# Kernel tuning notes

Hardware: AMD Instinct MI355X
Metric: run time of the kernel (lower is better)

The kernel has to match this reference:

```python
import jax, jax.numpy as jnp
import numpy as np

B, N, HD = 2, 2048, 2048
NH, KVH = 16, 4
D = HD // NH          # 128
R = NH // KVH         # 4 (kv_ratio)
KVD = KVH * D         # 512


def setup_inputs() -> dict:
    key = jax.random.key(0)
    ks = jax.random.split(key, 6)
    s = 0.02
    return {
        "tokens": jax.random.normal(ks[0], (B, N, HD), jnp.float32),
        "norm_w": jnp.ones((HD,), jnp.float32),
        "Wq": jax.random.normal(ks[1], (HD, HD), jnp.float32) * s,
        "bq": jnp.zeros((HD,), jnp.float32),
        "Wk": jax.random.normal(ks[2], (KVD, HD), jnp.float32) * s,
        "bk": jnp.zeros((KVD,), jnp.float32),
        "Wv": jax.random.normal(ks[3], (KVD, HD), jnp.float32) * s,
        "bv": jnp.zeros((KVD,), jnp.float32),
        "Wo": jax.random.normal(ks[4], (HD, HD), jnp.float32) * s,
        "bo": jnp.zeros((HD,), jnp.float32),
    }


def reference(tokens, norm_w, Wq, bq, Wk, bk, Wv, bv, Wo, bo):
    # RMSNorm (torch default eps=None -> finfo eps), learnable weight
    eps = jnp.finfo(tokens.dtype).eps
    x = tokens * jax.lax.rsqrt(jnp.mean(tokens * tokens, axis=-1, keepdims=True) + eps) * norm_w

    # projections -> [B, heads, N, D]
    q = (x @ Wq.T + bq).reshape(B, N, NH, D).transpose(0, 2, 1, 3)
    k = (x @ Wk.T + bk).reshape(B, N, KVH, D).transpose(0, 2, 1, 3)
    v = (x @ Wv.T + bv).reshape(B, N, KVH, D).transpose(0, 2, 1, 3)

    # GQA via tiling the kv block (matches torch.cat of copies: head h uses kv head h % KVH)
    k = jnp.tile(k, (1, R, 1, 1))
    v = jnp.tile(v, (1, R, 1, 1))

    # Faithful (inverted) mask: True where j <= i, and True positions are masked out.
    mask = jnp.arange(N)[None, :] <= jnp.arange(N)[:, None]  # [N, N]

    # No 1/sqrt(D) scaling in the original
    scores = jnp.einsum('bhid,bhjd->bhij', q, k)
    scores = jnp.where(mask[None, None, :, :], jnp.float32(-1e9), scores)
    attn = jax.nn.softmax(scores, axis=-1)

    a = jnp.einsum('bhij,bhjd->bhid', attn, v)       # [B, NH, N, D]
    a = a.transpose(0, 2, 1, 3).reshape(B, N, HD)    # [B, N, HD]
    return a @ Wo.T + bo
```

## Files before the change

### kernel.cpp

```cpp
#include <hip/hip_runtime.h>

#define BB   2
#define NN   2048
#define HDIM 2048
#define NHD  16
#define KVHD 4
#define DD   128
#define KVW  1024
#define MTOK (BB*NN)

typedef _Float16 h8 __attribute__((ext_vector_type(8)));
typedef _Float16 h4 __attribute__((ext_vector_type(4)));
typedef float    f4 __attribute__((ext_vector_type(4)));
typedef float    fx16 __attribute__((ext_vector_type(16)));
typedef short    b8 __attribute__((ext_vector_type(8)));

static __device__ __forceinline__ f4 mfma16(h8 a, h8 b, f4 c) {
    return __builtin_amdgcn_mfma_f32_16x16x32_f16(a, b, c, 0, 0, 0);
}
static __device__ __forceinline__ fx16 mfma32b(b8 a, b8 b, fx16 c) {
    return __builtin_amdgcn_mfma_f32_32x32x16_bf16(a, b, c, 0, 0, 0);
}

static __device__ __forceinline__ unsigned short f2bf(float f) {
    unsigned int u = __float_as_uint(f);
    u += 0x7FFF + ((u >> 16) & 1);
    return (unsigned short)(u >> 16);
}

static __device__ __forceinline__ void gload_lds16(const void* g, void* l) {
    __builtin_amdgcn_global_load_lds(
        (const __attribute__((address_space(1))) void*)g,
        (__attribute__((address_space(3))) void*)l, 16, 0, 0);
}

__global__ __launch_bounds__(256) void rmsnorm_k(const float* __restrict__ t,
                                                 const float* __restrict__ wn,
                                                 _Float16* __restrict__ xh) {
    const int row = blockIdx.x, tid = threadIdx.x;
    const float* rp = t + (size_t)row * HDIM;
    float4 v[2];
    float ss = 0.f;
    #pragma unroll
    for (int p = 0; p < 2; ++p) {
        float4 x = *(const float4*)(rp + (p * 256 + tid) * 4);
        v[p] = x;
        ss += x.x * x.x + x.y * x.y + x.z * x.z + x.w * x.w;
    }
    #pragma unroll
    for (int off = 32; off; off >>= 1) ss += __shfl_xor(ss, off, 64);
    __shared__ float sred[4];
    if ((tid & 63) == 0) sred[tid >> 6] = ss;
    __syncthreads();
    float rs = rsqrtf((sred[0] + sred[1] + sred[2] + sred[3]) * (1.0f / HDIM)
                      + 1.1920928955078125e-07f);
    _Float16* op = xh + (size_t)row * HDIM;
    #pragma unroll
    for (int p = 0; p < 2; ++p) {
        int base = (p * 256 + tid) * 4;
        float4 w = *(const float4*)(wn + base);
        h4 o;
        o[0] = (_Float16)(v[p].x * rs * w.x);
        o[1] = (_Float16)(v[p].y * rs * w.y);
        o[2] = (_Float16)(v[p].z * rs * w.z);
        o[3] = (_Float16)(v[p].w * rs * w.w);
        *(h4*)(op + base) = o;
    }
}

__global__ __launch_bounds__(256) void cvt_k(const float* __restrict__ src,
                                             _Float16* __restrict__ dst, int n) {
    int i = (blockIdx.x * 256 + threadIdx.x) * 4;
    if (i < n) {
        float4 v = *(const float4*)(src + i);
        h4 o; o[0] = (_Float16)v.x; o[1] = (_Float16)v.y;
        o[2] = (_Float16)v.z; o[3] = (_Float16)v.w;
        *(h4*)(dst + i) = o;
    }
}

__global__ void biascat_k(const float* __restrict__ bk, const float* __restrict__ bv,
                          float* __restrict__ bkv, float* __restrict__ vsum) {
    int i = blockIdx.x * 256 + threadIdx.x;
    bkv[i] = (i < 512) ? bk[i] : bv[i - 512];
    vsum[i] = 0.f;
}

__global__ __launch_bounds__(256) void vtrans_k(const _Float16* __restrict__ kv,
                                                unsigned short* __restrict__ vt) {
    const int tid = threadIdx.x;
    const int tok = blockIdx.x * 64 + (tid & 63);
    const int kvh = blockIdx.y;
    const int d0 = (tid >> 6) * 32;
    const int b = tok >> 11, n = tok & (NN - 1);
    const _Float16* src = kv + (size_t)tok * KVW + 512 + kvh * DD + d0;
    unsigned short* dstb = vt + ((size_t)(b * KVHD + kvh) * DD) * NN + n;
    #pragma unroll
    for (int u = 0; u < 4; ++u) {
        h8 v = *(const h8*)(src + u * 8);
        #pragma unroll
        for (int e = 0; e < 8; ++e)
            dstb[(size_t)(d0 + u * 8 + e) * NN] = f2bf((float)v[e]);
    }
}

template <int OUTF32>
__global__ __launch_bounds__(256, 2) void gemm_bt(const _Float16* __restrict__ A,
                                                  const _Float16* __restrict__ Bw,
                                                  const float* __restrict__ bias,
                                                  void* __restrict__ Cout,
                                                  int Ndim, int K) {
    __shared__ _Float16 sA[128 * 64];
    __shared__ _Float16 sB[128 * 64];
    const int tid = threadIdx.x;
    const int lane = tid & 63, w = tid >> 6;
    const int ln = lane & 15, quad = lane >> 4;
    const int wm = w >> 1, wn = w & 1;
    const int m0 = blockIdx.y * 128, n0 = blockIdx.x * 128;

    f4 acc[4][4] = {};
    for (int k0 = 0; k0 < K; k0 += 64) {
        #pragma unroll
        for (int it = 0; it < 4; ++it) {
            int chunk = it * 256 + tid;
            int row = chunk >> 3, p = chunk & 7;
            int c = p ^ (row & 7);
            gload_lds16(A + (size_t)(m0 + row) * K + k0 + c * 8, sA + chunk * 8);
            gload_lds16(Bw + (size_t)(n0 + row) * K + k0 + c * 8, sB + chunk * 8);
        }
        __syncthreads();
        #pragma unroll
        for (int kk = 0; kk < 2; ++kk) {
            h8 af[4], bf[4];
            #pragma unroll
            for (int mt = 0; mt < 4; ++mt)
                af[mt] = *(const h8*)&sA[(wm * 64 + mt * 16 + ln) * 64 +
                                         (((kk * 4 + quad) ^ (ln & 7)) << 3)];
            #pragma unroll
            for (int nt = 0; nt < 4; ++nt)
                bf[nt] = *(const h8*)&sB[(wn * 64 + nt * 16 + ln) * 64 +
                                         (((kk * 4 + quad) ^ (ln & 7)) << 3)];
            #pragma unroll
            for (int mt = 0; mt < 4; ++mt)
                #pragma unroll
                for (int nt = 0; nt < 4; ++nt)
                    acc[mt][nt] = mfma16(af[mt], bf[nt], acc[mt][nt]);
        }
        __syncthreads();
    }
    #pragma unroll
    for (int mt = 0; mt < 4; ++mt) {
        int rowb = m0 + wm * 64 + mt * 16 + quad * 4;
        #pragma unroll
        for (int nt = 0; nt < 4; ++nt) {
            int col = n0 + wn * 64 + nt * 16 + ln;
            float bv = bias[col];
            #pragma unroll
            for (int r = 0; r < 4; ++r) {
                float v = acc[mt][nt][r] + bv;
                if (OUTF32)
                    ((float*)Cout)[(size_t)(rowb + r) * Ndim + col] = v;
                else
                    ((_Float16*)Cout)[(size_t)(rowb + r) * Ndim + col] = (_Float16)v;
            }
        }
    }
}

__global__ __launch_bounds__(256, 2) void attn_k(const _Float16* __restrict__ qh,
                                                 const _Float16* __restrict__ kvp,
                                                 const unsigned short* __restrict__ vt,
                                                 _Float16* __restrict__ ah) {
    __shared__ _Float16 s_k[2][64 * 128];
    __shared__ unsigned short s_v[2][128 * 64];
    __shared__ unsigned short s_p[4][32 * 32];
    const int tid = threadIdx.x;
    const int lane = tid & 63, w = tid >> 6;
    const int ln = lane & 15, quad = lane >> 4;
    const int l5 = lane & 31, hi = lane >> 5;
    const int h = blockIdx.y, b = blockIdx.z;
    const int it0 = b ? (15 - (int)blockIdx.x) : (int)blockIdx.x;
    const int i0 = it0 * 128;
    const int kvh = h & 3;

    h8 qf[2][4];
    #pragma unroll
    for (int t = 0; t < 2; ++t) {
        const _Float16* qrow =
            qh + ((size_t)(b * NN + i0 + w * 32 + t * 16 + ln)) * HDIM + h * DD;
        #pragma unroll
        for (int kc = 0; kc < 4; ++kc)
            qf[t][kc] = *(const h8*)(qrow + kc * 32 + quad * 8);
    }

    b8 ones;
    #pragma unroll
    for (int e = 0; e < 8; ++e) ones[e] = (short)0x3F80;

    fx16 O[4] = {};
    fx16 OS = {};

    auto stage = [&](int jt, int bufi) {
        const int j0s = jt * 64;
        #pragma unroll
        for (int itr = 0; itr < 4; ++itr) {
            int chunk = itr * 256 + tid;
            int jj = chunk >> 4, p = chunk & 15;
            int c = p ^ (jj & 15);
            gload_lds16(kvp + ((size_t)(b * NN + j0s + jj)) * KVW + kvh * DD + c * 8,
                        &s_k[bufi][chunk * 8]);
        }
        #pragma unroll
        for (int itr = 0; itr < 4; ++itr) {
            int chunk = itr * 256 + tid;
            int d = chunk >> 3, p = chunk & 7;
            int c = p ^ (d & 7);
            gload_lds16(vt + ((size_t)(b * KVHD + kvh) * DD + d) * NN + j0s + c * 8,
                        &s_v[bufi][chunk * 8]);
        }
    };

    const int jt0 = it0 * 2;
    stage(jt0, 0);
    for (int jt = jt0; jt < 32; ++jt) {
        const int j0 = jt * 64;
        const int cur = (jt - jt0) & 1;
        __syncthreads();
        if (jt + 1 < 32) stage(jt + 1, cur ^ 1);

        f4 sc[2][4] = {};
        #pragma unroll
        for (int nt = 0; nt < 4; ++nt)
            #pragma unroll
            for (int kc = 0; kc < 4; ++kc) {
                h8 kf = *(const h8*)&s_k[cur][(nt * 16 + ln) * 128 +
                                              (((kc * 4 + quad) ^ ln) << 3)];
                sc[0][nt] = mfma16(kf, qf[0][kc], sc[0][nt]);
                sc[1][nt] = mfma16(kf, qf[1][kc], sc[1][nt]);
            }

        const bool need_mask = (jt < jt0 + 2);
        #pragma unroll
        for (int half = 0; half < 2; ++half) {
            #pragma unroll
            for (int t = 0; t < 2; ++t)
                #pragma unroll
                for (int nn = 0; nn < 2; ++nn) {
                    int nt = half * 2 + nn;
                    float pv[4];
                    #pragma unroll
                    for (int r = 0; r < 4; ++r) {
                        float s = sc[t][nt][r];
                        if (need_mask) {
                            int ig = i0 + w * 32 + t * 16 + ln;
                            int jg = j0 + nt * 16 + quad * 4 + r;
                            if (jg <= ig) s = -1e9f;
                        }
                        pv[r] = __expf(s);
                    }
                    unsigned int u0 = f2bf(pv[0]) | ((unsigned int)f2bf(pv[1]) << 16);
                    unsigned int u1 = f2bf(pv[2]) | ((unsigned int)f2bf(pv[3]) << 16);
                    int addr = (t * 16 + ln) * 32 +
                               (((nn * 2 + (quad >> 1)) ^ (ln & 3)) << 3) +
                               ((quad & 1) << 2);
                    *(uint2*)&s_p[w][addr] = make_uint2(u0, u1);
                }
            #pragma unroll
            for (int ks = 0; ks < 2; ++ks) {
                b8 ap = *(const b8*)&s_p[w][l5 * 32 +
                                            (((ks * 2 + hi) ^ (l5 & 3)) << 3)];
                #pragma unroll
                for (int nt4 = 0; nt4 < 4; ++nt4) {
                    b8 bv = *(const b8*)&s_v[cur][(nt4 * 32 + l5) * 64 +
                                                  (((half * 4 + ks * 2 + hi) ^ (l5 & 7)) << 3)];
                    O[nt4] = mfma32b(ap, bv, O[nt4]);
                }
                OS = mfma32b(ap, ones, OS);
            }
        }
    }

    float inv_l[16];
    #pragma unroll
    for (int rg = 0; rg < 16; ++rg) inv_l[rg] = 1.0f / OS[rg];
    #pragma unroll
    for (int nt4 = 0; nt4 < 4; ++nt4)
        #pragma unroll
        for (int rg = 0; rg < 16; ++rg) {
            int q = (rg & 3) + 8 * (rg >> 2) + 4 * hi;
            ah[((size_t)(b * NN + i0 + w * 32 + q)) * HDIM + h * DD + nt4 * 32 + l5] =
                (_Float16)(O[nt4][rg] * inv_l[rg]);
        }
}

__global__ __launch_bounds__(256) void vsum_k(const _Float16* __restrict__ kvp,
                                              float* __restrict__ vsum) {
    __shared__ float red[16][128];
    const int seg = blockIdx.x, kvh = blockIdx.y, b = blockIdx.z;
    const int tid = threadIdx.x;
    const int jj = tid >> 4, dc = (tid & 15) * 8;
    float acc[8] = {};
    #pragma unroll 4
    for (int j = seg * 256 + jj; j < seg * 256 + 256; j += 16) {
        h8 v = *(const h8*)(kvp + ((size_t)(b * NN + j)) * KVW + 512 + kvh * DD + dc);
        #pragma unroll
        for (int e = 0; e < 8; ++e) acc[e] += (float)v[e];
    }
    #pragma unroll
    for (int e = 0; e < 8; ++e) red[jj][dc + e] = acc[e];
    __syncthreads();
    if (tid < 128) {
        float s = 0.f;
        #pragma unroll
        for (int t = 0; t < 16; ++t) s += red[t][tid];
        atomicAdd(&vsum[(b * KVHD + kvh) * DD + tid], s);
    }
}

__global__ void fixup_write_k(const float* __restrict__ vsum,
                              _Float16* __restrict__ ah) {
    int b = blockIdx.x >> 2, kvh = blockIdx.x & 3, d = threadIdx.x;
    float mean = vsum[(b * KVHD + kvh) * DD + d] * (1.0f / NN);
    #pragma unroll
    for (int r = 0; r < 4; ++r) {
        int h = r * 4 + kvh;
        ah[((size_t)(b * NN + NN - 1)) * HDIM + h * DD + d] = (_Float16)mean;
    }
}

extern "C" void kernel_launch(void* const* d_in, const int* in_sizes, int n_in,
                              void* d_out, int out_size, void* d_ws, size_t ws_size,
                              hipStream_t stream) {
    const float* tokens = (const float*)d_in[0];
    const float* norm_w = (const float*)d_in[1];
    const float* Wq = (const float*)d_in[2];
    const float* bq = (const float*)d_in[3];
    const float* Wk = (const float*)d_in[4];
    const float* bk = (const float*)d_in[5];
    const float* Wv = (const float*)d_in[6];
    const float* bv = (const float*)d_in[7];
    const float* Wo = (const float*)d_in[8];
    const float* bo = (const float*)d_in[9];
    float* out = (float*)d_out;

    char* ws = (char*)d_ws;
    _Float16* x_h   = (_Float16*)(ws);
    _Float16* wq_h  = (_Float16*)(ws + 16777216);
    _Float16* wkv_h = (_Float16*)(ws + 25165824);
    _Float16* wo_h  = (_Float16*)(ws + 29360128);
    float*    bkv   = (float*)   (ws + 37748736);
    _Float16* q_h   = (_Float16*)(ws + 37752832);
    _Float16* kv_h  = (_Float16*)(ws + 54530048);
    _Float16* a_h   = (_Float16*)(ws + 62918656);
    unsigned short* vt_h = (unsigned short*)(ws + 79695872);
    float*    vsum  = (float*)   (ws + 81793024);

    rmsnorm_k<<<MTOK, 256, 0, stream>>>(tokens, norm_w, x_h);
    cvt_k<<<4096, 256, 0, stream>>>(Wq, wq_h, HDIM * HDIM);
    cvt_k<<<1024, 256, 0, stream>>>(Wk, wkv_h, 512 * HDIM);
    cvt_k<<<1024, 256, 0, stream>>>(Wv, wkv_h + 512 * HDIM, 512 * HDIM);
    cvt_k<<<4096, 256, 0, stream>>>(Wo, wo_h, HDIM * HDIM);
    biascat_k<<<4, 256, 0, stream>>>(bk, bv, bkv, vsum);

    gemm_bt<0><<<dim3(HDIM / 128, MTOK / 128), 256, 0, stream>>>(
        x_h, wq_h, bq, (void*)q_h, HDIM, HDIM);
    gemm_bt<0><<<dim3(KVW / 128, MTOK / 128), 256, 0, stream>>>(
        x_h, wkv_h, bkv, (void*)kv_h, KVW, HDIM);

    vtrans_k<<<dim3(MTOK / 64, KVHD), 256, 0, stream>>>(kv_h, vt_h);

    attn_k<<<dim3(16, NHD, BB), 256, 0, stream>>>(q_h, kv_h, vt_h, a_h);
    vsum_k<<<dim3(8, KVHD, BB), 256, 0, stream>>>(kv_h, vsum);
    fixup_write_k<<<BB * KVHD, 128, 0, stream>>>(vsum, a_h);

    gemm_bt<1><<<dim3(HDIM / 128, MTOK / 128), 256, 0, stream>>>(
        a_h, wo_h, bo, (void*)out, HDIM, HDIM);
}
```

Baseline: 319.6 us.

## Build P MFMA operands in registers via lane shuffles instead of LDS round-trip

The attention kernel no longer writes the exponentiated bf16 score tile to a per-wave shared buffer and reads it back as the A operand of the 32x32 MFMA. It packs probabilities in registers and exchanges half of them across lanes with a 16-lane xor shuffle to form the operand layout directly. It also reorders the P·V loop over 16-column key blocks. This removes LDS stores and loads and frees shared memory, at the cost of extra shuffles and selects. The vsum workspace offset also moves.

```diff
diff --git a/kernel.cpp b/kernel.cpp
--- a/kernel.cpp
+++ b/kernel.cpp
@@ -14,6 +14,7 @@
 typedef float    f4 __attribute__((ext_vector_type(4)));
 typedef float    fx16 __attribute__((ext_vector_type(16)));
 typedef short    b8 __attribute__((ext_vector_type(8)));
+typedef unsigned int u4v __attribute__((ext_vector_type(4)));
 
 static __device__ __forceinline__ f4 mfma16(h8 a, h8 b, f4 c) {
     return __builtin_amdgcn_mfma_f32_16x16x32_f16(a, b, c, 0, 0, 0);
@@ -173,11 +174,11 @@
                                                  _Float16* __restrict__ ah) {
     __shared__ _Float16 s_k[2][64 * 128];
     __shared__ unsigned short s_v[2][128 * 64];
-    __shared__ unsigned short s_p[4][32 * 32];
     const int tid = threadIdx.x;
     const int lane = tid & 63, w = tid >> 6;
     const int ln = lane & 15, quad = lane >> 4;
     const int l5 = lane & 31, hi = lane >> 5;
+    const int sel = quad & 1;
     const int h = blockIdx.y, b = blockIdx.z;
     const int it0 = b ? (15 - (int)blockIdx.x) : (int)blockIdx.x;
     const int i0 = it0 * 128;
@@ -240,43 +241,54 @@
             }
 
         const bool need_mask = (jt < jt0 + 2);
-        #pragma unroll
-        for (int half = 0; half < 2; ++half) {
-            #pragma unroll
-            for (int t = 0; t < 2; ++t)
-                #pragma unroll
-                for (int nn = 0; nn < 2; ++nn) {
-                    int nt = half * 2 + nn;
-                    float pv[4];
-                    #pragma unroll
-                    for (int r = 0; r < 4; ++r) {
-                        float s = sc[t][nt][r];
-                        if (need_mask) {
-                            int ig = i0 + w * 32 + t * 16 + ln;
-                            int jg = j0 + nt * 16 + quad * 4 + r;
-                            if (jg <= ig) s = -1e9f;
-                        }
-                        pv[r] = __expf(s);
-                    }
-                    unsigned int u0 = f2bf(pv[0]) | ((unsigned int)f2bf(pv[1]) << 16);
-                    unsigned int u1 = f2bf(pv[2]) | ((unsigned int)f2bf(pv[3]) << 16);
-                    int addr = (t * 16 + ln) * 32 +
-                               (((nn * 2 + (quad >> 1)) ^ (ln & 3)) << 3) +
-                               ((quad & 1) << 2);
-                    *(uint2*)&s_p[w][addr] = make_uint2(u0, u1);
+        unsigned int u0[4][2], u1[4][2];
+        #pragma unroll
+        for (int nt = 0; nt < 4; ++nt)
+            #pragma unroll
+            for (int rr = 0; rr < 2; ++rr) {
+                float a0 = sc[0][nt][2 * rr], a1 = sc[0][nt][2 * rr + 1];
+                float c0 = sc[1][nt][2 * rr], c1 = sc[1][nt][2 * rr + 1];
+                if (need_mask) {
+                    int jg = j0 + nt * 16 + quad * 4 + 2 * rr;
+                    int ig0 = i0 + w * 32 + ln;
+                    int ig1 = ig0 + 16;
+                    if (jg <= ig0) a0 = -1e9f;
+                    if (jg + 1 <= ig0) a1 = -1e9f;
+                    if (jg <= ig1) c0 = -1e9f;
+                    if (jg + 1 <= ig1) c1 = -1e9f;
                 }
-            #pragma unroll
-            for (int ks = 0; ks < 2; ++ks) {
-                b8 ap = *(const b8*)&s_p[w][l5 * 32 +
-                                            (((ks * 2 + hi) ^ (l5 & 3)) << 3)];
-                #pragma unroll
-                for (int nt4 = 0; nt4 < 4; ++nt4) {
-                    b8 bv = *(const b8*)&s_v[cur][(nt4 * 32 + l5) * 64 +
-                                                  (((half * 4 + ks * 2 + hi) ^ (l5 & 7)) << 3)];
-                    O[nt4] = mfma32b(ap, bv, O[nt4]);
-                }
-                OS = mfma32b(ap, ones, OS);
+                u0[nt][rr] = (unsigned int)f2bf(__expf(a0)) |
+                             ((unsigned int)f2bf(__expf(a1)) << 16);
+                u1[nt][rr] = (unsigned int)f2bf(__expf(c0)) |
+                             ((unsigned int)f2bf(__expf(c1)) << 16);
             }
+
+        b8 paf[4];
+        #pragma unroll
+        for (int nt = 0; nt < 4; ++nt) {
+            unsigned int own0 = sel ? u1[nt][0] : u0[nt][0];
+            unsigned int own1 = sel ? u1[nt][1] : u0[nt][1];
+            unsigned int oth0 = sel ? u0[nt][0] : u1[nt][0];
+            unsigned int oth1 = sel ? u0[nt][1] : u1[nt][1];
+            unsigned int r0 = __shfl_xor(oth0, 16, 64);
+            unsigned int r1 = __shfl_xor(oth1, 16, 64);
+            u4v pw;
+            pw[0] = sel ? r0 : own0;
+            pw[1] = sel ? r1 : own1;
+            pw[2] = sel ? own0 : r0;
+            pw[3] = sel ? own1 : r1;
+            paf[nt] = __builtin_bit_cast(b8, pw);
+        }
+
+        #pragma unroll
+        for (int nt = 0; nt < 4; ++nt) {
+            #pragma unroll
+            for (int dblk = 0; dblk < 4; ++dblk) {
+                b8 bv = *(const b8*)&s_v[cur][(dblk * 32 + l5) * 64 +
+                                              (((nt * 2 + hi) ^ (l5 & 7)) << 3)];
+                O[dblk] = mfma32b(paf[nt], bv, O[dblk]);
+            }
+            OS = mfma32b(paf[nt], ones, OS);
         }
     }
 
@@ -353,7 +365,7 @@
     _Float16* kv_h  = (_Float16*)(ws + 54530048);
     _Float16* a_h   = (_Float16*)(ws + 62918656);
     unsigned short* vt_h = (unsigned short*)(ws + 79695872);
-    float*    vsum  = (float*)   (ws + 81793024);
+    float*    vsum  = (float*)   (ws + 83890176);
 
     rmsnorm_k<<<MTOK, 256, 0, stream>>>(tokens, norm_w, x_h);
     cvt_k<<<4096, 256, 0, stream>>>(Wq, wq_h, HDIM * HDIM);
```

Measured after the change: 325.7 us. No clear change (+1.9%).
